# Performance work log

Hardware: AMD Instinct MI355X
Metric: run time of the kernel (lower is better)

The kernel has to match this reference:

```python
import jax, jax.numpy as jnp
import numpy as np
import math

T, B, C, F, H, LF, GF = 1024, 8, 512, 64, 8, 64, 64


def setup_inputs() -> dict:
    key = jax.random.key(0)
    ks = jax.random.split(key, 24)
    s = 0.02  # weight init scale for stability through the recurrence
    rn = lambda k, shp, sc=1.0: jax.random.normal(k, shp, jnp.float32) * sc
    inp = {
        "x": rn(ks[0], (B, T, C)),
        "ln_g": jnp.ones((C,), jnp.float32),
        "ln_b": jnp.zeros((C,), jnp.float32),
        "tl_initial": rn(ks[1], (C,)),
        "tl_premix": jax.random.uniform(ks[2], (C,), jnp.float32),
        "tl_w1": rn(ks[3], (C, LF), s), "tl_b1": jnp.zeros((LF,), jnp.float32),
        "tl_w2": rn(ks[4], (LF, C), s), "tl_b2": jnp.zeros((C,), jnp.float32),
        "bias": jnp.zeros((C,), jnp.float32),
        "gating_res": jax.random.uniform(ks[5], (C,), jnp.float32),
        "g_w1": rn(ks[6], (C, GF), s), "g_b1": jnp.zeros((GF,), jnp.float32),
        "g_w2": rn(ks[7], (GF, C), s), "g_b2": jnp.zeros((C,), jnp.float32),
        "dn_initial": rn(ks[8], (H, F, F)),
        "A_w": rn(ks[9], (H, C, F), s), "A_b": rn(ks[10], (H, F), s),
        "B_w": jnp.zeros((H, C, F), jnp.float32), "B_b": rn(ks[11], (H, F), s),
        "C_w": rn(ks[12], (H, C, F), s), "C_b": rn(ks[13], (H, F), s),
        "D_w": rn(ks[14], (H, C, F), s), "D_b": rn(ks[15], (H, F), s),
        "I_w": rn(ks[16], (H, C, F), s), "I_b": rn(ks[17], (H, F), s),
        "S_w": rn(ks[18], (H, C, F), s), "S_b": rn(ks[19], (H, F), s),
        "O_w": rn(ks[20], (H, F, C), s),
    }
    return inp


def _deltanet_head(y, init_state, Aw, Ab, Bw, Bb, Cw, Cb, Dw, Db, Iw, Ib, Sw, Sb, Ow):
    # y: [T, B, C]; init_state: [F, F]
    f = init_state.shape[-1]
    sf = math.sqrt(f)  # awk_safe
    a = y @ Aw + Ab   # [T,B,F]
    b = y @ Bw + Bb
    c = y @ Cw + Cb
    d = y @ Dw + Db
    i = y @ Iw + Ib
    sel = y @ Sw + Sb
    st0 = jnp.broadcast_to(init_state, (y.shape[1], f, f)).astype(y.dtype)

    def step(st, ins):
        sel_t, a_t, b_t, c_t, d_t, i_t = ins  # each [B,F]
        st = (st * jax.nn.sigmoid(i_t)[:, None, :]
              + jnp.einsum('bij,bj->bi', st, a_t)[:, :, None] * b_t[:, None, :] / sf
              + c_t[:, :, None] * d_t[:, None, :])
        out = jnp.einsum('bf,bfg->bg', sel_t, st)
        return st, out

    st, o = jax.lax.scan(step, st0, (sel, a, b, c, d, i))
    return o @ Ow, st  # [T,B,C]


def reference(x, ln_g, ln_b, tl_initial, tl_premix, tl_w1, tl_b1, tl_w2, tl_b2,
              bias, gating_res, g_w1, g_b1, g_w2, g_b2, dn_initial,
              A_w, A_b, B_w, B_b, C_w, C_b, D_w, D_b, I_w, I_b, S_w, S_b, O_w):
    xt = jnp.swapaxes(x, 0, -2)  # [T, B, C] (time_dim=-2)
    res = xt
    # LayerNorm (eps=1e-5)
    mu = jnp.mean(xt, -1, keepdims=True)
    var = jnp.mean((xt - mu) ** 2, -1, keepdims=True)
    h = (xt - mu) / jnp.sqrt(var + 1e-5) * ln_g + ln_b
    # TokenLerp (state=None -> xf[0]=initial)
    xf = jnp.concatenate([jnp.broadcast_to(tl_initial, (1,) + h.shape[1:]).astype(h.dtype), h[:-1]], axis=0)
    pm = h + (xf - h) * tl_premix
    decide = jax.nn.sigmoid(jax.nn.gelu(pm @ tl_w1 + tl_b1, approximate=False) @ tl_w2 + tl_b2)
    h = h + (xf - h) * decide
    # y starts from bias; heads are chained sequentially (y feeds next head)
    y = jnp.broadcast_to(bias, h.shape).astype(h.dtype)
    for k in range(dn_initial.shape[0]):
        y, _ = _deltanet_head(y, dn_initial[k], A_w[k], A_b[k], B_w[k], B_b[k],
                              C_w[k], C_b[k], D_w[k], D_b[k], I_w[k], I_b[k],
                              S_w[k], S_b[k], O_w[k])
    gate = jax.nn.sigmoid(jax.nn.gelu((y + h * gating_res) @ g_w1 + g_b1, approximate=False) @ g_w2 + g_b2)
    # use_residual=True path: returns res + y (no transpose back, matching source)
    return res + y * gate
```

## Files before the change

kernel.cpp:

```cpp
#include <hip/hip_runtime.h>
#include <hip/hip_bf16.h>

#define T_DIM 1024
#define B_DIM 8
#define C_DIM 512
#define F_DIM 64
#define H_DIM 8
#define CHUNK 32
#define NCHUNK 32

__device__ __forceinline__ float sigmoidf_(float v) { return 1.0f / (1.0f + __expf(-v)); }
__device__ __forceinline__ float geluf_(float v) { return 0.5f * v * (1.0f + erff(v * 0.70710678118654752f)); }
__device__ __forceinline__ float rl_(float v, int l) {
  return __uint_as_float(__builtin_amdgcn_readlane(__float_as_uint(v), l));
}

struct GemmArgs {
  const float* A; const float* W; const float* bias; float* out;
  int M, K, N;
  const float* x; const float* mu; const float* rstd;
  const float* ln_g; const float* ln_b; const float* tl_initial; const float* premix;
  const float* yv; const float* gres;
  float* h2;
  const float* Wg[6]; const float* bg[6];
};

struct AFetch {
  float4 v0, v1, v2, v3, v4;
  float s0, s1, s2, s3;
};

template<int MODE_A>
__device__ __forceinline__ AFetch a_fetch(const GemmArgs& g, int r, int c) {
  AFetch f; f.s0 = f.s1 = f.s2 = f.s3 = 0.f;
  if (MODE_A == 0) {
    f.v0 = *(const float4*)&g.A[r * g.K + c];
  } else if (MODE_A == 1) {
    const int b = r & 7, t = r >> 3;
    f.v0 = *(const float4*)&g.x[(b * T_DIM + t) * C_DIM + c];
    f.s0 = g.mu[r]; f.s1 = g.rstd[r];
    if (t > 0) {
      f.v1 = *(const float4*)&g.x[(b * T_DIM + t - 1) * C_DIM + c];
      f.s2 = g.mu[r - 8]; f.s3 = g.rstd[r - 8];
    } else {
      f.v1 = *(const float4*)&g.tl_initial[c];
    }
    f.v2 = *(const float4*)&g.ln_g[c];
    f.v3 = *(const float4*)&g.ln_b[c];
    f.v4 = *(const float4*)&g.premix[c];
  } else {
    f.v0 = *(const float4*)&g.yv[(r >> 3) * C_DIM + c];
    f.v1 = *(const float4*)&g.h2[r * C_DIM + c];
    f.v2 = *(const float4*)&g.gres[c];
  }
  return f;
}

template<int MODE_A>
__device__ __forceinline__ float4 a_combine(const AFetch& f, int r) {
  if (MODE_A == 0) return f.v0;
  float4 o;
  float* op = (float*)&o;
  const float* xa = (const float*)&f.v0;
  const float* xb = (const float*)&f.v1;
  const float* lg = (const float*)&f.v2;
  const float* lb = (const float*)&f.v3;
  const float* pm = (const float*)&f.v4;
  if (MODE_A == 1) {
    const int t = r >> 3;
    #pragma unroll
    for (int q = 0; q < 4; ++q) {
      float h  = (xa[q] - f.s0) * f.s1 * lg[q] + lb[q];
      float xf = (t == 0) ? xb[q] : (xb[q] - f.s2) * f.s3 * lg[q] + lb[q];
      op[q] = h + (xf - h) * pm[q];
    }
    return o;
  }
  #pragma unroll
  for (int q = 0; q < 4; ++q)
    op[q] = xa[q] + xb[q] * lg[q];
  return o;
}

template<int MODE_B>
__device__ __forceinline__ float4 w_fetch(const GemmArgs& g, int kk, int n0, int tc) {
  if (MODE_B == 1)
    return *(const float4*)&g.Wg[blockIdx.y][kk * 64 + (tc << 2)];
  return *(const float4*)&g.W[kk * g.N + n0 + (tc << 2)];
}

template<int MODE_A, int MODE_B, int EPI>
__global__ __launch_bounds__(256) void gemm_kernel(GemmArgs g) {
  __shared__ float AsT[16][68];
  __shared__ float Bs[16][64];
  const int m0 = blockIdx.x * 64, n0 = blockIdx.y * 64;
  const int tid = threadIdx.x;
  const int tr = tid >> 4, tc = tid & 15;
  const int ai = tid >> 2, aj = (tid & 3) << 2;
  const float scg = (MODE_B == 1 && blockIdx.y == 1) ? 0.125f : 1.0f;
  float acc[4][4] = {};
  AFetch fa = a_fetch<MODE_A>(g, m0 + ai, aj);
  float4 wv = w_fetch<MODE_B>(g, tr, n0, tc);
  for (int k0 = 0; k0 < g.K; k0 += 16) {
    if (k0) __syncthreads();
    const float4 av = a_combine<MODE_A>(fa, m0 + ai);
    AsT[aj + 0][ai] = av.x;
    AsT[aj + 1][ai] = av.y;
    AsT[aj + 2][ai] = av.z;
    AsT[aj + 3][ai] = av.w;
    *(float4*)&Bs[tr][tc << 2] =
        make_float4(wv.x * scg, wv.y * scg, wv.z * scg, wv.w * scg);
    if (k0 + 16 < g.K) {
      fa = a_fetch<MODE_A>(g, m0 + ai, k0 + 16 + aj);
      wv = w_fetch<MODE_B>(g, k0 + 16 + tr, n0, tc);
    }
    __syncthreads();
    #pragma unroll
    for (int kk = 0; kk < 16; ++kk) {
      const float4 a4 = *(const float4*)&AsT[kk][tr << 2];
      const float4 b4 = *(const float4*)&Bs[kk][tc << 2];
      const float avr[4] = {a4.x, a4.y, a4.z, a4.w};
      const float bvr[4] = {b4.x, b4.y, b4.z, b4.w};
      #pragma unroll
      for (int r_ = 0; r_ < 4; ++r_)
        #pragma unroll
        for (int c_ = 0; c_ < 4; ++c_)
          acc[r_][c_] = fmaf(avr[r_], bvr[c_], acc[r_][c_]);
    }
  }
  #pragma unroll
  for (int r_ = 0; r_ < 4; ++r_) {
    const int rr = m0 + (tr << 2) + r_;
    #pragma unroll
    for (int c_ = 0; c_ < 4; ++c_) {
      const int lc = (tc << 2) + c_;
      const int cc = n0 + lc;
      float v = acc[r_][c_];
      if (MODE_B == 1) v += g.bg[blockIdx.y][lc] * scg;
      else if (g.bias) v += g.bias[cc];
      if (EPI == 0) {
        g.out[rr * g.N + cc] = v;
      } else if (EPI == 1) {
        g.out[rr * g.N + cc] = geluf_(v);
      } else if (EPI == 2) {
        float d = sigmoidf_(v);
        const int b = rr & 7, t = rr >> 3;
        float xv = g.x[(b * T_DIM + t) * C_DIM + cc];
        float h = (xv - g.mu[rr]) * g.rstd[rr] * g.ln_g[cc] + g.ln_b[cc];
        float xf;
        if (t == 0) xf = g.tl_initial[cc];
        else {
          float xp = g.x[(b * T_DIM + t - 1) * C_DIM + cc];
          xf = (xp - g.mu[rr - 8]) * g.rstd[rr - 8] * g.ln_g[cc] + g.ln_b[cc];
        }
        g.h2[rr * C_DIM + cc] = h + (xf - h) * d;
      } else {
        float gate = sigmoidf_(v);
        const int b = rr & 7, t = rr >> 3;
        float res = g.x[(b * T_DIM + t) * C_DIM + cc];
        g.out[rr * C_DIM + cc] = res + g.yv[t * C_DIM + cc] * gate;
      }
    }
  }
}

__global__ __launch_bounds__(256) void ln_stats_kernel(const float* __restrict__ x,
                                                       float* __restrict__ mu,
                                                       float* __restrict__ rstd) {
  const int row = blockIdx.x * 4 + (threadIdx.x >> 6);
  const int lane = threadIdx.x & 63;
  const int b = row & 7, t = row >> 3;
  const float* xr = x + (b * T_DIM + t) * C_DIM;
  float4 v0 = *(const float4*)&xr[lane * 8];
  float4 v1 = *(const float4*)&xr[lane * 8 + 4];
  float s  = v0.x + v0.y + v0.z + v0.w + v1.x + v1.y + v1.z + v1.w;
  float s2 = v0.x*v0.x + v0.y*v0.y + v0.z*v0.z + v0.w*v0.w
           + v1.x*v1.x + v1.y*v1.y + v1.z*v1.z + v1.w*v1.w;
  #pragma unroll
  for (int m = 1; m < 64; m <<= 1) { s += __shfl_xor(s, m); s2 += __shfl_xor(s2, m); }
  if (lane == 0) {
    float mean = s * (1.0f / 512.0f);
    float var = s2 * (1.0f / 512.0f) - mean * mean;
    mu[row] = mean;
    rstd[row] = rsqrtf(var + 1e-5f);
  }
}

__global__ __launch_bounds__(256) void yinit_kernel(const float* __restrict__ bias,
                                                    float* __restrict__ y) {
  int i = blockIdx.x * blockDim.x + threadIdx.x;
  y[i] = bias[i & (C_DIM - 1)];
}


__global__ __launch_bounds__(256) void scan_phaseA(const float* __restrict__ PRJ,
                                                   float* __restrict__ chPT,
                                                   float* __restrict__ chS) {
  const int j = blockIdx.x;
  const int tid = threadIdx.x;
  const int ri = tid >> 4, ci = tid & 15;
  float Pm[4][4], Sm[4][4];
  #pragma unroll
  for (int r = 0; r < 4; ++r)
    #pragma unroll
    for (int c = 0; c < 4; ++c) {
      Pm[r][c] = (ri * 4 + r == ci * 4 + c) ? 1.0f : 0.0f;
      Sm[r][c] = 0.0f;
    }
  const float* base = PRJ + j * CHUNK * 384;
  float4 pa = *(const float4*)&base[      ci * 4];
  float4 pb = *(const float4*)&base[ 64 + ci * 4];
  float4 pc = *(const float4*)&base[128 + ri * 4];
  float4 pd = *(const float4*)&base[192 + ci * 4];
  float4 pi = *(const float4*)&base[256 + ci * 4];
  for (int s = 0; s < CHUNK; ++s) {
    float4 na = pa, nb = pb, nc2 = pc, nd = pd, ni = pi;
    if (s + 1 < CHUNK) {
      const float* b2 = base + (s + 1) * 384;
      na  = *(const float4*)&b2[      ci * 4];
      nb  = *(const float4*)&b2[ 64 + ci * 4];
      nc2 = *(const float4*)&b2[128 + ri * 4];
      nd  = *(const float4*)&b2[192 + ci * 4];
      ni  = *(const float4*)&b2[256 + ci * 4];
    }
    const float sg[4] = {sigmoidf_(pi.x), sigmoidf_(pi.y), sigmoidf_(pi.z), sigmoidf_(pi.w)};
    const float aa[4] = {pa.x, pa.y, pa.z, pa.w};
    const float bb[4] = {pb.x, pb.y, pb.z, pb.w};
    const float cv[4] = {pc.x, pc.y, pc.z, pc.w};
    const float dd[4] = {pd.x, pd.y, pd.z, pd.w};
    float rp[4], rs[4];
    #pragma unroll
    for (int r = 0; r < 4; ++r) {
      rp[r] = Pm[r][0]*aa[0] + Pm[r][1]*aa[1] + Pm[r][2]*aa[2] + Pm[r][3]*aa[3];
      rs[r] = Sm[r][0]*aa[0] + Sm[r][1]*aa[1] + Sm[r][2]*aa[2] + Sm[r][3]*aa[3];
    }
    #pragma unroll
    for (int m = 1; m <= 8; m <<= 1) {
      #pragma unroll
      for (int r = 0; r < 4; ++r) {
        rp[r] += __shfl_xor(rp[r], m);
        rs[r] += __shfl_xor(rs[r], m);
      }
    }
    #pragma unroll
    for (int r = 0; r < 4; ++r)
      #pragma unroll
      for (int c = 0; c < 4; ++c) {
        Pm[r][c] = Pm[r][c] * sg[c] + rp[r] * bb[c];
        Sm[r][c] = Sm[r][c] * sg[c] + rs[r] * bb[c] + cv[r] * dd[c];
      }
    pa = na; pb = nb; pc = nc2; pd = nd; pi = ni;
  }
  float* cpT = chPT + j * 4096;
  float* cs  = chS + j * 4096;
  #pragma unroll
  for (int c = 0; c < 4; ++c)
    *(float4*)&cpT[(ci*4+c)*64 + ri*4] =
        make_float4(Pm[0][c], Pm[1][c], Pm[2][c], Pm[3][c]);
  #pragma unroll
  for (int r = 0; r < 4; ++r)
    *(float4*)&cs[(ri*4+r)*64 + ci*4] = make_float4(Sm[r][0], Sm[r][1], Sm[r][2], Sm[r][3]);
}

__device__ __forceinline__ float cstep(const float4 (&P)[16], float sv, float rv) {
  float p0 = 0.f, p1 = 0.f, p2 = 0.f, p3 = 0.f;
  #pragma unroll
  for (int q = 0; q < 16; ++q) {
    p0 = fmaf(rl_(rv, q * 4 + 0), P[q].x, p0);
    p1 = fmaf(rl_(rv, q * 4 + 1), P[q].y, p1);
    p2 = fmaf(rl_(rv, q * 4 + 2), P[q].z, p2);
    p3 = fmaf(rl_(rv, q * 4 + 3), P[q].w, p3);
  }
  return sv + ((p0 + p1) + (p2 + p3));
}

__global__ __launch_bounds__(64) void scan_combine(const float* __restrict__ st0,
                                                   const float* __restrict__ chPT,
                                                   const float* __restrict__ chS,
                                                   float* __restrict__ bnd) {
  const int lane = threadIdx.x;
  const int r = blockIdx.x;
  float rv = st0[r * 64 + lane];
  const float* basePT = chPT + lane * 64;
  const float* baseS  = chS + r * 64 + lane;
  float* bndRL = bnd + r * 64 + lane;
  for (int j = 0; j < NCHUNK; ++j) {
    float4 P[16];
    const float* pp = basePT + j * 4096;
    #pragma unroll
    for (int q = 0; q < 16; ++q) P[q] = *(const float4*)&pp[q * 4];
    const float sv = baseS[j * 4096];
    bndRL[j * 4096] = rv;
    rv = cstep(P, sv, rv);
  }
}

__global__ __launch_bounds__(256) void scan_phaseC(const float* __restrict__ PRJ,
                                                   const float* __restrict__ bnd,
                                                   const float* __restrict__ Ow,
                                                   float* __restrict__ y) {
  __shared__ float olds[CHUNK][4][64];
  __shared__ float osT[64][CHUNK + 1];
  const int j = blockIdx.x;
  const int tid = threadIdx.x;
  const int ri = tid >> 4, ci = tid & 15, w = tid >> 6;
  float st[4][4];
  #pragma unroll
  for (int r = 0; r < 4; ++r) {
    const float4 v = *(const float4*)&bnd[j*4096 + (ri*4+r)*64 + ci*4];
    st[r][0] = v.x; st[r][1] = v.y; st[r][2] = v.z; st[r][3] = v.w;
  }
  const float* base = PRJ + j * CHUNK * 384;
  float4 pa = *(const float4*)&base[      ci * 4];
  float4 pb = *(const float4*)&base[ 64 + ci * 4];
  float4 pc = *(const float4*)&base[128 + ri * 4];
  float4 pd = *(const float4*)&base[192 + ci * 4];
  float4 pi = *(const float4*)&base[256 + ci * 4];
  float4 ps = *(const float4*)&base[320 + ri * 4];
  for (int s = 0; s < CHUNK; ++s) {
    float4 na = pa, nb = pb, nc2 = pc, nd = pd, ni = pi, ns = ps;
    if (s + 1 < CHUNK) {
      const float* b2 = base + (s + 1) * 384;
      na  = *(const float4*)&b2[      ci * 4];
      nb  = *(const float4*)&b2[ 64 + ci * 4];
      nc2 = *(const float4*)&b2[128 + ri * 4];
      nd  = *(const float4*)&b2[192 + ci * 4];
      ni  = *(const float4*)&b2[256 + ci * 4];
      ns  = *(const float4*)&b2[320 + ri * 4];
    }
    const float sg[4] = {sigmoidf_(pi.x), sigmoidf_(pi.y), sigmoidf_(pi.z), sigmoidf_(pi.w)};
    const float aa[4] = {pa.x, pa.y, pa.z, pa.w};
    const float bb[4] = {pb.x, pb.y, pb.z, pb.w};
    const float cv[4] = {pc.x, pc.y, pc.z, pc.w};
    const float dd[4] = {pd.x, pd.y, pd.z, pd.w};
    const float ss[4] = {ps.x, ps.y, ps.z, ps.w};
    float rd[4];
    #pragma unroll
    for (int r = 0; r < 4; ++r)
      rd[r] = st[r][0]*aa[0] + st[r][1]*aa[1] + st[r][2]*aa[2] + st[r][3]*aa[3];
    #pragma unroll
    for (int m = 1; m <= 8; m <<= 1) {
      #pragma unroll
      for (int r = 0; r < 4; ++r) rd[r] += __shfl_xor(rd[r], m);
    }
    float po[4] = {0.f, 0.f, 0.f, 0.f};
    #pragma unroll
    for (int r = 0; r < 4; ++r)
      #pragma unroll
      for (int c = 0; c < 4; ++c) {
        const float nv = st[r][c] * sg[c] + rd[r] * bb[c] + cv[r] * dd[c];
        st[r][c] = nv;
        po[c] = fmaf(ss[r], nv, po[c]);
      }
    #pragma unroll
    for (int c = 0; c < 4; ++c) {
      po[c] += __shfl_xor(po[c], 16);
      po[c] += __shfl_xor(po[c], 32);
    }
    if ((tid & 48) == 0)
      *(float4*)&olds[s][w][ci * 4] = make_float4(po[0], po[1], po[2], po[3]);
    pa = na; pb = nb; pc = nc2; pd = nd; pi = ni; ps = ns;
  }
  __syncthreads();
  #pragma unroll
  for (int e = 0; e < 8; ++e) {
    const int id = tid + 256 * e;
    const int f = id & 63, t = id >> 6;
    osT[f][t] = olds[t][0][f] + olds[t][1][f] + olds[t][2][f] + olds[t][3][f];
  }
  __syncthreads();
  const int c0 = tid << 1;
  float2 acc[CHUNK];
  #pragma unroll
  for (int t = 0; t < CHUNK; ++t) acc[t] = make_float2(0.f, 0.f);
  #pragma unroll 1
  for (int fo = 0; fo < 8; ++fo) {
    float2 ow[8];
    #pragma unroll
    for (int q = 0; q < 8; ++q)
      ow[q] = *(const float2*)&Ow[(fo * 8 + q) * C_DIM + c0];
    #pragma unroll
    for (int q = 0; q < 8; ++q) {
      const int f = fo * 8 + q;
      #pragma unroll
      for (int t8 = 0; t8 < 8; ++t8) {
        const float4 ov = *(const float4*)&osT[f][t8 * 4];
        acc[t8*4+0].x = fmaf(ov.x, ow[q].x, acc[t8*4+0].x);
        acc[t8*4+0].y = fmaf(ov.x, ow[q].y, acc[t8*4+0].y);
        acc[t8*4+1].x = fmaf(ov.y, ow[q].x, acc[t8*4+1].x);
        acc[t8*4+1].y = fmaf(ov.y, ow[q].y, acc[t8*4+1].y);
        acc[t8*4+2].x = fmaf(ov.z, ow[q].x, acc[t8*4+2].x);
        acc[t8*4+2].y = fmaf(ov.z, ow[q].y, acc[t8*4+2].y);
        acc[t8*4+3].x = fmaf(ov.w, ow[q].x, acc[t8*4+3].x);
        acc[t8*4+3].y = fmaf(ov.w, ow[q].y, acc[t8*4+3].y);
      }
    }
  }
  #pragma unroll
  for (int t = 0; t < CHUNK; ++t)
    *(float2*)&y[(j * CHUNK + t) * C_DIM + c0] = acc[t];
}

extern "C" void kernel_launch(void* const* d_in, const int* in_sizes, int n_in,
                              void* d_out, int out_size, void* d_ws, size_t ws_size,
                              hipStream_t stream) {
  const float* x       = (const float*)d_in[0];
  const float* ln_g    = (const float*)d_in[1];
  const float* ln_b    = (const float*)d_in[2];
  const float* tl_init = (const float*)d_in[3];
  const float* premix  = (const float*)d_in[4];
  const float* tl_w1   = (const float*)d_in[5];
  const float* tl_b1   = (const float*)d_in[6];
  const float* tl_w2   = (const float*)d_in[7];
  const float* tl_b2   = (const float*)d_in[8];
  const float* bias    = (const float*)d_in[9];
  const float* gres    = (const float*)d_in[10];
  const float* g_w1    = (const float*)d_in[11];
  const float* g_b1    = (const float*)d_in[12];
  const float* g_w2    = (const float*)d_in[13];
  const float* g_b2    = (const float*)d_in[14];
  const float* dn_init = (const float*)d_in[15];
  const float* A_w     = (const float*)d_in[16];
  const float* A_b     = (const float*)d_in[17];
  const float* B_w     = (const float*)d_in[18];
  const float* B_b     = (const float*)d_in[19];
  const float* C_w     = (const float*)d_in[20];
  const float* C_b     = (const float*)d_in[21];
  const float* D_w     = (const float*)d_in[22];
  const float* D_b     = (const float*)d_in[23];
  const float* I_w     = (const float*)d_in[24];
  const float* I_b     = (const float*)d_in[25];
  const float* S_w     = (const float*)d_in[26];
  const float* S_b     = (const float*)d_in[27];
  const float* O_w     = (const float*)d_in[28];

  float* ws      = (float*)d_ws;
  float* mu      = ws;
  float* rstd    = mu + 8192;
  float* hidden1 = rstd + 8192;
  float* y       = hidden1 + 524288;
  float* PRJ     = y + 524288;
  float* chPT    = PRJ + 393216;
  float* chS     = chPT + 131072;
  float* bnd     = chS + 131072;
  float* h2      = (float*)d_out;

  ln_stats_kernel<<<2048, 256, 0, stream>>>(x, mu, rstd);
  yinit_kernel<<<2048, 256, 0, stream>>>(bias, y);

  GemmArgs ga = {};
  ga.x = x; ga.mu = mu; ga.rstd = rstd; ga.ln_g = ln_g; ga.ln_b = ln_b;
  ga.tl_initial = tl_init; ga.premix = premix; ga.gres = gres; ga.h2 = h2;

  {
    GemmArgs g = ga; g.W = tl_w1; g.bias = tl_b1; g.out = hidden1;
    g.M = 8192; g.K = 512; g.N = 64;
    gemm_kernel<1, 0, 1><<<dim3(128, 1), 256, 0, stream>>>(g);
  }
  {
    GemmArgs g = ga; g.A = hidden1; g.W = tl_w2; g.bias = tl_b2;
    g.M = 8192; g.K = 64; g.N = 512;
    gemm_kernel<0, 0, 2><<<dim3(128, 8), 256, 0, stream>>>(g);
  }

  for (int k = 0; k < H_DIM; ++k) {
    {
      GemmArgs g = ga; g.A = y; g.out = PRJ; g.M = 1024; g.K = 512; g.N = 384;
      const int woff = k * C_DIM * F_DIM, boff = k * F_DIM;
      g.Wg[0] = A_w + woff; g.Wg[1] = B_w + woff; g.Wg[2] = C_w + woff;
      g.Wg[3] = D_w + woff; g.Wg[4] = I_w + woff; g.Wg[5] = S_w + woff;
      g.bg[0] = A_b + boff; g.bg[1] = B_b + boff; g.bg[2] = C_b + boff;
      g.bg[3] = D_b + boff; g.bg[4] = I_b + boff; g.bg[5] = S_b + boff;
      gemm_kernel<0, 1, 0><<<dim3(16, 6), 256, 0, stream>>>(g);
    }
    scan_phaseA<<<NCHUNK, 256, 0, stream>>>(PRJ, chPT, chS);
    scan_combine<<<64, 64, 0, stream>>>(dn_init + k * 4096, chPT, chS, bnd);
    scan_phaseC<<<NCHUNK, 256, 0, stream>>>(PRJ, bnd, O_w + k * F_DIM * C_DIM, y);
  }

  {
    GemmArgs g = ga; g.yv = y; g.W = g_w1; g.bias = g_b1; g.out = hidden1;
    g.M = 8192; g.K = 512; g.N = 64;
    gemm_kernel<2, 0, 1><<<dim3(128, 1), 256, 0, stream>>>(g);
  }
  {
    GemmArgs g = ga; g.yv = y; g.A = hidden1; g.W = g_w2; g.bias = g_b2;
    g.out = (float*)d_out; g.M = 8192; g.K = 64; g.N = 512;
    gemm_kernel<0, 0, 3><<<dim3(128, 8), 256, 0, stream>>>(g);
  }
}
```

Baseline: 968.0 us.

## Fuse per-head projection and chunked scan phases into one cooperative persistent kernel

Replaces the 32 per-head kernel launches (projection GEMM, chunk scan, combine, output phase) and the y-init kernel with a single cooperative kernel of 96 blocks that loops over heads and uses grid-wide syncs between phases. This is meant to remove launch overhead and the gaps between small, latency-bound kernels in the sequential head chain. In exchange, grid.sync costs are added, and many blocks sit idle during the scan phases. The generic GEMM template also drops its multi-weight mode.

```diff
diff --git a/kernel.cpp b/kernel.cpp
--- a/kernel.cpp
+++ b/kernel.cpp
@@ -1,5 +1,8 @@
 #include <hip/hip_runtime.h>
 #include <hip/hip_bf16.h>
+#include <hip/hip_cooperative_groups.h>
+
+namespace cg = cooperative_groups;
 
 #define T_DIM 1024
 #define B_DIM 8
@@ -22,7 +25,6 @@
   const float* ln_g; const float* ln_b; const float* tl_initial; const float* premix;
   const float* yv; const float* gres;
   float* h2;
-  const float* Wg[6]; const float* bg[6];
 };
 
 struct AFetch {
@@ -82,14 +84,7 @@
   return o;
 }
 
-template<int MODE_B>
-__device__ __forceinline__ float4 w_fetch(const GemmArgs& g, int kk, int n0, int tc) {
-  if (MODE_B == 1)
-    return *(const float4*)&g.Wg[blockIdx.y][kk * 64 + (tc << 2)];
-  return *(const float4*)&g.W[kk * g.N + n0 + (tc << 2)];
-}
-
-template<int MODE_A, int MODE_B, int EPI>
+template<int MODE_A, int EPI>
 __global__ __launch_bounds__(256) void gemm_kernel(GemmArgs g) {
   __shared__ float AsT[16][68];
   __shared__ float Bs[16][64];
@@ -97,10 +92,9 @@
   const int tid = threadIdx.x;
   const int tr = tid >> 4, tc = tid & 15;
   const int ai = tid >> 2, aj = (tid & 3) << 2;
-  const float scg = (MODE_B == 1 && blockIdx.y == 1) ? 0.125f : 1.0f;
   float acc[4][4] = {};
   AFetch fa = a_fetch<MODE_A>(g, m0 + ai, aj);
-  float4 wv = w_fetch<MODE_B>(g, tr, n0, tc);
+  float4 wv = *(const float4*)&g.W[tr * g.N + n0 + (tc << 2)];
   for (int k0 = 0; k0 < g.K; k0 += 16) {
     if (k0) __syncthreads();
     const float4 av = a_combine<MODE_A>(fa, m0 + ai);
@@ -108,11 +102,10 @@
     AsT[aj + 1][ai] = av.y;
     AsT[aj + 2][ai] = av.z;
     AsT[aj + 3][ai] = av.w;
-    *(float4*)&Bs[tr][tc << 2] =
-        make_float4(wv.x * scg, wv.y * scg, wv.z * scg, wv.w * scg);
+    *(float4*)&Bs[tr][tc << 2] = wv;
     if (k0 + 16 < g.K) {
       fa = a_fetch<MODE_A>(g, m0 + ai, k0 + 16 + aj);
-      wv = w_fetch<MODE_B>(g, k0 + 16 + tr, n0, tc);
+      wv = *(const float4*)&g.W[(k0 + 16 + tr) * g.N + n0 + (tc << 2)];
     }
     __syncthreads();
     #pragma unroll
@@ -133,14 +126,10 @@
     const int rr = m0 + (tr << 2) + r_;
     #pragma unroll
     for (int c_ = 0; c_ < 4; ++c_) {
-      const int lc = (tc << 2) + c_;
-      const int cc = n0 + lc;
+      const int cc = n0 + (tc << 2) + c_;
       float v = acc[r_][c_];
-      if (MODE_B == 1) v += g.bg[blockIdx.y][lc] * scg;
-      else if (g.bias) v += g.bias[cc];
-      if (EPI == 0) {
-        g.out[rr * g.N + cc] = v;
-      } else if (EPI == 1) {
+      if (g.bias) v += g.bias[cc];
+      if (EPI == 1) {
         g.out[rr * g.N + cc] = geluf_(v);
       } else if (EPI == 2) {
         float d = sigmoidf_(v);
@@ -186,82 +175,6 @@
   }
 }
 
-__global__ __launch_bounds__(256) void yinit_kernel(const float* __restrict__ bias,
-                                                    float* __restrict__ y) {
-  int i = blockIdx.x * blockDim.x + threadIdx.x;
-  y[i] = bias[i & (C_DIM - 1)];
-}
-
-
-__global__ __launch_bounds__(256) void scan_phaseA(const float* __restrict__ PRJ,
-                                                   float* __restrict__ chPT,
-                                                   float* __restrict__ chS) {
-  const int j = blockIdx.x;
-  const int tid = threadIdx.x;
-  const int ri = tid >> 4, ci = tid & 15;
-  float Pm[4][4], Sm[4][4];
-  #pragma unroll
-  for (int r = 0; r < 4; ++r)
-    #pragma unroll
-    for (int c = 0; c < 4; ++c) {
-      Pm[r][c] = (ri * 4 + r == ci * 4 + c) ? 1.0f : 0.0f;
-      Sm[r][c] = 0.0f;
-    }
-  const float* base = PRJ + j * CHUNK * 384;
-  float4 pa = *(const float4*)&base[      ci * 4];
-  float4 pb = *(const float4*)&base[ 64 + ci * 4];
-  float4 pc = *(const float4*)&base[128 + ri * 4];
-  float4 pd = *(const float4*)&base[192 + ci * 4];
-  float4 pi = *(const float4*)&base[256 + ci * 4];
-  for (int s = 0; s < CHUNK; ++s) {
-    float4 na = pa, nb = pb, nc2 = pc, nd = pd, ni = pi;
-    if (s + 1 < CHUNK) {
-      const float* b2 = base + (s + 1) * 384;
-      na  = *(const float4*)&b2[      ci * 4];
-      nb  = *(const float4*)&b2[ 64 + ci * 4];
-      nc2 = *(const float4*)&b2[128 + ri * 4];
-      nd  = *(const float4*)&b2[192 + ci * 4];
-      ni  = *(const float4*)&b2[256 + ci * 4];
-    }
-    const float sg[4] = {sigmoidf_(pi.x), sigmoidf_(pi.y), sigmoidf_(pi.z), sigmoidf_(pi.w)};
-    const float aa[4] = {pa.x, pa.y, pa.z, pa.w};
-    const float bb[4] = {pb.x, pb.y, pb.z, pb.w};
-    const float cv[4] = {pc.x, pc.y, pc.z, pc.w};
-    const float dd[4] = {pd.x, pd.y, pd.z, pd.w};
-    float rp[4], rs[4];
-    #pragma unroll
-    for (int r = 0; r < 4; ++r) {
-      rp[r] = Pm[r][0]*aa[0] + Pm[r][1]*aa[1] + Pm[r][2]*aa[2] + Pm[r][3]*aa[3];
-      rs[r] = Sm[r][0]*aa[0] + Sm[r][1]*aa[1] + Sm[r][2]*aa[2] + Sm[r][3]*aa[3];
-    }
-    #pragma unroll
-    for (int m = 1; m <= 8; m <<= 1) {
-      #pragma unroll
-      for (int r = 0; r < 4; ++r) {
-        rp[r] += __shfl_xor(rp[r], m);
-        rs[r] += __shfl_xor(rs[r], m);
-      }
-    }
-    #pragma unroll
-    for (int r = 0; r < 4; ++r)
-      #pragma unroll
-      for (int c = 0; c < 4; ++c) {
-        Pm[r][c] = Pm[r][c] * sg[c] + rp[r] * bb[c];
-        Sm[r][c] = Sm[r][c] * sg[c] + rs[r] * bb[c] + cv[r] * dd[c];
-      }
-    pa = na; pb = nb; pc = nc2; pd = nd; pi = ni;
-  }
-  float* cpT = chPT + j * 4096;
-  float* cs  = chS + j * 4096;
-  #pragma unroll
-  for (int c = 0; c < 4; ++c)
-    *(float4*)&cpT[(ci*4+c)*64 + ri*4] =
-        make_float4(Pm[0][c], Pm[1][c], Pm[2][c], Pm[3][c]);
-  #pragma unroll
-  for (int r = 0; r < 4; ++r)
-    *(float4*)&cs[(ri*4+r)*64 + ci*4] = make_float4(Sm[r][0], Sm[r][1], Sm[r][2], Sm[r][3]);
-}
-
 __device__ __forceinline__ float cstep(const float4 (&P)[16], float sv, float rv) {
   float p0 = 0.f, p1 = 0.f, p2 = 0.f, p3 = 0.f;
   #pragma unroll
@@ -274,131 +187,265 @@
   return sv + ((p0 + p1) + (p2 + p3));
 }
 
-__global__ __launch_bounds__(64) void scan_combine(const float* __restrict__ st0,
-                                                   const float* __restrict__ chPT,
-                                                   const float* __restrict__ chS,
-                                                   float* __restrict__ bnd) {
-  const int lane = threadIdx.x;
-  const int r = blockIdx.x;
-  float rv = st0[r * 64 + lane];
-  const float* basePT = chPT + lane * 64;
-  const float* baseS  = chS + r * 64 + lane;
-  float* bndRL = bnd + r * 64 + lane;
-  for (int j = 0; j < NCHUNK; ++j) {
-    float4 P[16];
-    const float* pp = basePT + j * 4096;
-    #pragma unroll
-    for (int q = 0; q < 16; ++q) P[q] = *(const float4*)&pp[q * 4];
-    const float sv = baseS[j * 4096];
-    bndRL[j * 4096] = rv;
-    rv = cstep(P, sv, rv);
-  }
-}
-
-__global__ __launch_bounds__(256) void scan_phaseC(const float* __restrict__ PRJ,
-                                                   const float* __restrict__ bnd,
-                                                   const float* __restrict__ Ow,
-                                                   float* __restrict__ y) {
-  __shared__ float olds[CHUNK][4][64];
-  __shared__ float osT[64][CHUNK + 1];
-  const int j = blockIdx.x;
+struct HeadArgs {
+  const float* bias;
+  const float* dn_init;
+  const float* Ws[6];
+  const float* bs[6];
+  const float* Ow;
+  float* y; float* PRJ; float* chPT; float* chS; float* bnd;
+};
+
+__global__ __launch_bounds__(256) void head_loop_kernel(HeadArgs a) {
+  cg::grid_group grid = cg::this_grid();
+  __shared__ float smem[10304];
+  const int blk = blockIdx.x;
   const int tid = threadIdx.x;
-  const int ri = tid >> 4, ci = tid & 15, w = tid >> 6;
-  float st[4][4];
-  #pragma unroll
-  for (int r = 0; r < 4; ++r) {
-    const float4 v = *(const float4*)&bnd[j*4096 + (ri*4+r)*64 + ci*4];
-    st[r][0] = v.x; st[r][1] = v.y; st[r][2] = v.z; st[r][3] = v.w;
-  }
-  const float* base = PRJ + j * CHUNK * 384;
-  float4 pa = *(const float4*)&base[      ci * 4];
-  float4 pb = *(const float4*)&base[ 64 + ci * 4];
-  float4 pc = *(const float4*)&base[128 + ri * 4];
-  float4 pd = *(const float4*)&base[192 + ci * 4];
-  float4 pi = *(const float4*)&base[256 + ci * 4];
-  float4 ps = *(const float4*)&base[320 + ri * 4];
-  for (int s = 0; s < CHUNK; ++s) {
-    float4 na = pa, nb = pb, nc2 = pc, nd = pd, ni = pi, ns = ps;
-    if (s + 1 < CHUNK) {
-      const float* b2 = base + (s + 1) * 384;
-      na  = *(const float4*)&b2[      ci * 4];
-      nb  = *(const float4*)&b2[ 64 + ci * 4];
-      nc2 = *(const float4*)&b2[128 + ri * 4];
-      nd  = *(const float4*)&b2[192 + ci * 4];
-      ni  = *(const float4*)&b2[256 + ci * 4];
-      ns  = *(const float4*)&b2[320 + ri * 4];
-    }
-    const float sg[4] = {sigmoidf_(pi.x), sigmoidf_(pi.y), sigmoidf_(pi.z), sigmoidf_(pi.w)};
-    const float aa[4] = {pa.x, pa.y, pa.z, pa.w};
-    const float bb[4] = {pb.x, pb.y, pb.z, pb.w};
-    const float cv[4] = {pc.x, pc.y, pc.z, pc.w};
-    const float dd[4] = {pd.x, pd.y, pd.z, pd.w};
-    const float ss[4] = {ps.x, ps.y, ps.z, ps.w};
-    float rd[4];
-    #pragma unroll
-    for (int r = 0; r < 4; ++r)
-      rd[r] = st[r][0]*aa[0] + st[r][1]*aa[1] + st[r][2]*aa[2] + st[r][3]*aa[3];
-    #pragma unroll
-    for (int m = 1; m <= 8; m <<= 1) {
-      #pragma unroll
-      for (int r = 0; r < 4; ++r) rd[r] += __shfl_xor(rd[r], m);
-    }
-    float po[4] = {0.f, 0.f, 0.f, 0.f};
-    #pragma unroll
-    for (int r = 0; r < 4; ++r)
-      #pragma unroll
-      for (int c = 0; c < 4; ++c) {
-        const float nv = st[r][c] * sg[c] + rd[r] * bb[c] + cv[r] * dd[c];
-        st[r][c] = nv;
-        po[c] = fmaf(ss[r], nv, po[c]);
-      }
-    #pragma unroll
-    for (int c = 0; c < 4; ++c) {
-      po[c] += __shfl_xor(po[c], 16);
-      po[c] += __shfl_xor(po[c], 32);
-    }
-    if ((tid & 48) == 0)
-      *(float4*)&olds[s][w][ci * 4] = make_float4(po[0], po[1], po[2], po[3]);
-    pa = na; pb = nb; pc = nc2; pd = nd; pi = ni; ps = ns;
-  }
-  __syncthreads();
-  #pragma unroll
-  for (int e = 0; e < 8; ++e) {
-    const int id = tid + 256 * e;
-    const int f = id & 63, t = id >> 6;
-    osT[f][t] = olds[t][0][f] + olds[t][1][f] + olds[t][2][f] + olds[t][3][f];
-  }
-  __syncthreads();
-  const int c0 = tid << 1;
-  float2 acc[CHUNK];
-  #pragma unroll
-  for (int t = 0; t < CHUNK; ++t) acc[t] = make_float2(0.f, 0.f);
-  #pragma unroll 1
-  for (int fo = 0; fo < 8; ++fo) {
-    float2 ow[8];
-    #pragma unroll
-    for (int q = 0; q < 8; ++q)
-      ow[q] = *(const float2*)&Ow[(fo * 8 + q) * C_DIM + c0];
-    #pragma unroll
-    for (int q = 0; q < 8; ++q) {
-      const int f = fo * 8 + q;
-      #pragma unroll
-      for (int t8 = 0; t8 < 8; ++t8) {
-        const float4 ov = *(const float4*)&osT[f][t8 * 4];
-        acc[t8*4+0].x = fmaf(ov.x, ow[q].x, acc[t8*4+0].x);
-        acc[t8*4+0].y = fmaf(ov.x, ow[q].y, acc[t8*4+0].y);
-        acc[t8*4+1].x = fmaf(ov.y, ow[q].x, acc[t8*4+1].x);
-        acc[t8*4+1].y = fmaf(ov.y, ow[q].y, acc[t8*4+1].y);
-        acc[t8*4+2].x = fmaf(ov.z, ow[q].x, acc[t8*4+2].x);
-        acc[t8*4+2].y = fmaf(ov.z, ow[q].y, acc[t8*4+2].y);
-        acc[t8*4+3].x = fmaf(ov.w, ow[q].x, acc[t8*4+3].x);
-        acc[t8*4+3].y = fmaf(ov.w, ow[q].y, acc[t8*4+3].y);
-      }
-    }
-  }
-  #pragma unroll
-  for (int t = 0; t < CHUNK; ++t)
-    *(float2*)&y[(j * CHUNK + t) * C_DIM + c0] = acc[t];
+
+  for (int i = blk * 256 + tid; i < T_DIM * C_DIM; i += 96 * 256)
+    a.y[i] = a.bias[i & (C_DIM - 1)];
+  grid.sync();
+
+  for (int k = 0; k < H_DIM; ++k) {
+    {
+      const int m0 = (blk & 15) * 64, grp = blk >> 4;
+      float (*AsT)[68] = (float(*)[68])smem;
+      float (*Bs)[64] = (float(*)[64])(smem + 16 * 68);
+      const int tr = tid >> 4, tc = tid & 15;
+      const int ai = tid >> 2, aj = (tid & 3) << 2;
+      const float* W = a.Ws[grp] + k * (C_DIM * F_DIM);
+      const float scg = (grp == 1) ? 0.125f : 1.0f;
+      float acc[4][4] = {};
+      float4 fa = *(const float4*)&a.y[(m0 + ai) * C_DIM + aj];
+      float4 wv = *(const float4*)&W[tr * 64 + (tc << 2)];
+      for (int k0 = 0; k0 < C_DIM; k0 += 16) {
+        if (k0) __syncthreads();
+        AsT[aj + 0][ai] = fa.x; AsT[aj + 1][ai] = fa.y;
+        AsT[aj + 2][ai] = fa.z; AsT[aj + 3][ai] = fa.w;
+        *(float4*)&Bs[tr][tc << 2] =
+            make_float4(wv.x * scg, wv.y * scg, wv.z * scg, wv.w * scg);
+        if (k0 + 16 < C_DIM) {
+          fa = *(const float4*)&a.y[(m0 + ai) * C_DIM + k0 + 16 + aj];
+          wv = *(const float4*)&W[(k0 + 16 + tr) * 64 + (tc << 2)];
+        }
+        __syncthreads();
+        #pragma unroll
+        for (int kk = 0; kk < 16; ++kk) {
+          const float4 a4 = *(const float4*)&AsT[kk][tr << 2];
+          const float4 b4 = *(const float4*)&Bs[kk][tc << 2];
+          const float avr[4] = {a4.x, a4.y, a4.z, a4.w};
+          const float bvr[4] = {b4.x, b4.y, b4.z, b4.w};
+          #pragma unroll
+          for (int r_ = 0; r_ < 4; ++r_)
+            #pragma unroll
+            for (int c_ = 0; c_ < 4; ++c_)
+              acc[r_][c_] = fmaf(avr[r_], bvr[c_], acc[r_][c_]);
+        }
+      }
+      const float* bb = a.bs[grp] + k * F_DIM;
+      #pragma unroll
+      for (int r_ = 0; r_ < 4; ++r_) {
+        const int rr = m0 + (tr << 2) + r_;
+        #pragma unroll
+        for (int c_ = 0; c_ < 4; ++c_) {
+          const int lc = (tc << 2) + c_;
+          a.PRJ[rr * 384 + grp * 64 + lc] = acc[r_][c_] + bb[lc] * scg;
+        }
+      }
+    }
+    grid.sync();
+
+    if (blk < NCHUNK) {
+      const int j = blk;
+      const int ri = tid >> 4, ci = tid & 15;
+      float Pm[4][4], Sm[4][4];
+      #pragma unroll
+      for (int r = 0; r < 4; ++r)
+        #pragma unroll
+        for (int c = 0; c < 4; ++c) {
+          Pm[r][c] = (ri * 4 + r == ci * 4 + c) ? 1.0f : 0.0f;
+          Sm[r][c] = 0.0f;
+        }
+      const float* base = a.PRJ + j * CHUNK * 384;
+      float4 pa = *(const float4*)&base[      ci * 4];
+      float4 pb = *(const float4*)&base[ 64 + ci * 4];
+      float4 pc = *(const float4*)&base[128 + ri * 4];
+      float4 pd = *(const float4*)&base[192 + ci * 4];
+      float4 pi = *(const float4*)&base[256 + ci * 4];
+      for (int s = 0; s < CHUNK; ++s) {
+        float4 na = pa, nb = pb, nc2 = pc, nd = pd, ni = pi;
+        if (s + 1 < CHUNK) {
+          const float* b2 = base + (s + 1) * 384;
+          na  = *(const float4*)&b2[      ci * 4];
+          nb  = *(const float4*)&b2[ 64 + ci * 4];
+          nc2 = *(const float4*)&b2[128 + ri * 4];
+          nd  = *(const float4*)&b2[192 + ci * 4];
+          ni  = *(const float4*)&b2[256 + ci * 4];
+        }
+        const float sg[4] = {sigmoidf_(pi.x), sigmoidf_(pi.y), sigmoidf_(pi.z), sigmoidf_(pi.w)};
+        const float aa[4] = {pa.x, pa.y, pa.z, pa.w};
+        const float bb2[4] = {pb.x, pb.y, pb.z, pb.w};
+        const float cv[4] = {pc.x, pc.y, pc.z, pc.w};
+        const float dd[4] = {pd.x, pd.y, pd.z, pd.w};
+        float rp[4], rs[4];
+        #pragma unroll
+        for (int r = 0; r < 4; ++r) {
+          rp[r] = Pm[r][0]*aa[0] + Pm[r][1]*aa[1] + Pm[r][2]*aa[2] + Pm[r][3]*aa[3];
+          rs[r] = Sm[r][0]*aa[0] + Sm[r][1]*aa[1] + Sm[r][2]*aa[2] + Sm[r][3]*aa[3];
+        }
+        #pragma unroll
+        for (int m = 1; m <= 8; m <<= 1) {
+          #pragma unroll
+          for (int r = 0; r < 4; ++r) {
+            rp[r] += __shfl_xor(rp[r], m);
+            rs[r] += __shfl_xor(rs[r], m);
+          }
+        }
+        #pragma unroll
+        for (int r = 0; r < 4; ++r)
+          #pragma unroll
+          for (int c = 0; c < 4; ++c) {
+            Pm[r][c] = Pm[r][c] * sg[c] + rp[r] * bb2[c];
+            Sm[r][c] = Sm[r][c] * sg[c] + rs[r] * bb2[c] + cv[r] * dd[c];
+          }
+        pa = na; pb = nb; pc = nc2; pd = nd; pi = ni;
+      }
+      float* cpT = a.chPT + j * 4096;
+      float* cs  = a.chS + j * 4096;
+      #pragma unroll
+      for (int c = 0; c < 4; ++c)
+        *(float4*)&cpT[(ci*4+c)*64 + ri*4] =
+            make_float4(Pm[0][c], Pm[1][c], Pm[2][c], Pm[3][c]);
+      #pragma unroll
+      for (int r = 0; r < 4; ++r)
+        *(float4*)&cs[(ri*4+r)*64 + ci*4] =
+            make_float4(Sm[r][0], Sm[r][1], Sm[r][2], Sm[r][3]);
+    }
+    grid.sync();
+
+    if (blk < 16) {
+      const int lane = tid & 63;
+      const int r = blk * 4 + (tid >> 6);
+      float rv = a.dn_init[k * 4096 + r * 64 + lane];
+      const float* basePT = a.chPT + lane * 64;
+      const float* baseS  = a.chS + r * 64 + lane;
+      float* bndRL = a.bnd + r * 64 + lane;
+      for (int j = 0; j < NCHUNK; ++j) {
+        float4 P[16];
+        const float* pp = basePT + j * 4096;
+        #pragma unroll
+        for (int q = 0; q < 16; ++q) P[q] = *(const float4*)&pp[q * 4];
+        const float sv = baseS[j * 4096];
+        bndRL[j * 4096] = rv;
+        rv = cstep(P, sv, rv);
+      }
+    }
+    grid.sync();
+
+    if (blk < NCHUNK) {
+      const int j = blk;
+      float (*olds)[4][64] = (float(*)[4][64])smem;
+      float (*osT)[CHUNK + 1] = (float(*)[CHUNK + 1])(smem + 8192);
+      const int ri = tid >> 4, ci = tid & 15, w = tid >> 6;
+      const float* Ow = a.Ow + k * F_DIM * C_DIM;
+      float st[4][4];
+      #pragma unroll
+      for (int r = 0; r < 4; ++r) {
+        const float4 v = *(const float4*)&a.bnd[j*4096 + (ri*4+r)*64 + ci*4];
+        st[r][0] = v.x; st[r][1] = v.y; st[r][2] = v.z; st[r][3] = v.w;
+      }
+      const float* base = a.PRJ + j * CHUNK * 384;
+      float4 pa = *(const float4*)&base[      ci * 4];
+      float4 pb = *(const float4*)&base[ 64 + ci * 4];
+      float4 pc = *(const float4*)&base[128 + ri * 4];
+      float4 pd = *(const float4*)&base[192 + ci * 4];
+      float4 pi = *(const float4*)&base[256 + ci * 4];
+      float4 ps = *(const float4*)&base[320 + ri * 4];
+      for (int s = 0; s < CHUNK; ++s) {
+        float4 na = pa, nb = pb, nc2 = pc, nd = pd, ni = pi, ns = ps;
+        if (s + 1 < CHUNK) {
+          const float* b2 = base + (s + 1) * 384;
+          na  = *(const float4*)&b2[      ci * 4];
+          nb  = *(const float4*)&b2[ 64 + ci * 4];
+          nc2 = *(const float4*)&b2[128 + ri * 4];
+          nd  = *(const float4*)&b2[192 + ci * 4];
+          ni  = *(const float4*)&b2[256 + ci * 4];
+          ns  = *(const float4*)&b2[320 + ri * 4];
+        }
+        const float sg[4] = {sigmoidf_(pi.x), sigmoidf_(pi.y), sigmoidf_(pi.z), sigmoidf_(pi.w)};
+        const float aa[4] = {pa.x, pa.y, pa.z, pa.w};
+        const float bb2[4] = {pb.x, pb.y, pb.z, pb.w};
+        const float cv[4] = {pc.x, pc.y, pc.z, pc.w};
+        const float dd[4] = {pd.x, pd.y, pd.z, pd.w};
+        const float ss[4] = {ps.x, ps.y, ps.z, ps.w};
+        float rd[4];
+        #pragma unroll
+        for (int r = 0; r < 4; ++r)
+          rd[r] = st[r][0]*aa[0] + st[r][1]*aa[1] + st[r][2]*aa[2] + st[r][3]*aa[3];
+        #pragma unroll
+        for (int m = 1; m <= 8; m <<= 1) {
+          #pragma unroll
+          for (int r = 0; r < 4; ++r) rd[r] += __shfl_xor(rd[r], m);
+        }
+        float po[4] = {0.f, 0.f, 0.f, 0.f};
+        #pragma unroll
+        for (int r = 0; r < 4; ++r)
+          #pragma unroll
+          for (int c = 0; c < 4; ++c) {
+            const float nv = st[r][c] * sg[c] + rd[r] * bb2[c] + cv[r] * dd[c];
+            st[r][c] = nv;
+            po[c] = fmaf(ss[r], nv, po[c]);
+          }
+        #pragma unroll
+        for (int c = 0; c < 4; ++c) {
+          po[c] += __shfl_xor(po[c], 16);
+          po[c] += __shfl_xor(po[c], 32);
+        }
+        if ((tid & 48) == 0)
+          *(float4*)&olds[s][w][ci * 4] = make_float4(po[0], po[1], po[2], po[3]);
+        pa = na; pb = nb; pc = nc2; pd = nd; pi = ni; ps = ns;
+      }
+      __syncthreads();
+      #pragma unroll
+      for (int e = 0; e < 8; ++e) {
+        const int id = tid + 256 * e;
+        const int f = id & 63, t = id >> 6;
+        osT[f][t] = olds[t][0][f] + olds[t][1][f] + olds[t][2][f] + olds[t][3][f];
+      }
+      __syncthreads();
+      const int c0 = tid << 1;
+      float2 acc[CHUNK];
+      #pragma unroll
+      for (int t = 0; t < CHUNK; ++t) acc[t] = make_float2(0.f, 0.f);
+      #pragma unroll 1
+      for (int fo = 0; fo < 8; ++fo) {
+        float2 ow[8];
+        #pragma unroll
+        for (int q = 0; q < 8; ++q)
+          ow[q] = *(const float2*)&Ow[(fo * 8 + q) * C_DIM + c0];
+        #pragma unroll
+        for (int q = 0; q < 8; ++q) {
+          const int f = fo * 8 + q;
+          #pragma unroll
+          for (int t8 = 0; t8 < 8; ++t8) {
+            const float4 ov = *(const float4*)&osT[f][t8 * 4];
+            acc[t8*4+0].x = fmaf(ov.x, ow[q].x, acc[t8*4+0].x);
+            acc[t8*4+0].y = fmaf(ov.x, ow[q].y, acc[t8*4+0].y);
+            acc[t8*4+1].x = fmaf(ov.y, ow[q].x, acc[t8*4+1].x);
+            acc[t8*4+1].y = fmaf(ov.y, ow[q].y, acc[t8*4+1].y);
+            acc[t8*4+2].x = fmaf(ov.z, ow[q].x, acc[t8*4+2].x);
+            acc[t8*4+2].y = fmaf(ov.z, ow[q].y, acc[t8*4+2].y);
+            acc[t8*4+3].x = fmaf(ov.w, ow[q].x, acc[t8*4+3].x);
+            acc[t8*4+3].y = fmaf(ov.w, ow[q].y, acc[t8*4+3].y);
+          }
+        }
+      }
+      #pragma unroll
+      for (int t = 0; t < CHUNK; ++t)
+        *(float2*)&a.y[(j * CHUNK + t) * C_DIM + c0] = acc[t];
+    }
+    grid.sync();
+  }
 }
 
 extern "C" void kernel_launch(void* const* d_in, const int* in_sizes, int n_in,
@@ -446,7 +493,6 @@
   float* h2      = (float*)d_out;
 
   ln_stats_kernel<<<2048, 256, 0, stream>>>(x, mu, rstd);
-  yinit_kernel<<<2048, 256, 0, stream>>>(bias, y);
 
   GemmArgs ga = {};
   ga.x = x; ga.mu = mu; ga.rstd = rstd; ga.ln_g = ln_g; ga.ln_b = ln_b;
@@ -455,37 +501,35 @@
   {
     GemmArgs g = ga; g.W = tl_w1; g.bias = tl_b1; g.out = hidden1;
     g.M = 8192; g.K = 512; g.N = 64;
-    gemm_kernel<1, 0, 1><<<dim3(128, 1), 256, 0, stream>>>(g);
+    gemm_kernel<1, 1><<<dim3(128, 1), 256, 0, stream>>>(g);
   }
   {
     GemmArgs g = ga; g.A = hidden1; g.W = tl_w2; g.bias = tl_b2;
     g.M = 8192; g.K = 64; g.N = 512;
-    gemm_kernel<0, 0, 2><<<dim3(128, 8), 256, 0, stream>>>(g);
-  }
-
-  for (int k = 0; k < H_DIM; ++k) {
-    {
-      GemmArgs g = ga; g.A = y; g.out = PRJ; g.M = 1024; g.K = 512; g.N = 384;
-      const int woff = k * C_DIM * F_DIM, boff = k * F_DIM;
-      g.Wg[0] = A_w + woff; g.Wg[1] = B_w + woff; g.Wg[2] = C_w + woff;
-      g.Wg[3] = D_w + woff; g.Wg[4] = I_w + woff; g.Wg[5] = S_w + woff;
-      g.bg[0] = A_b + boff; g.bg[1] = B_b + boff; g.bg[2] = C_b + boff;
-      g.bg[3] = D_b + boff; g.bg[4] = I_b + boff; g.bg[5] = S_b + boff;
-      gemm_kernel<0, 1, 0><<<dim3(16, 6), 256, 0, stream>>>(g);
-    }
-    scan_phaseA<<<NCHUNK, 256, 0, stream>>>(PRJ, chPT, chS);
-    scan_combine<<<64, 64, 0, stream>>>(dn_init + k * 4096, chPT, chS, bnd);
-    scan_phaseC<<<NCHUNK, 256, 0, stream>>>(PRJ, bnd, O_w + k * F_DIM * C_DIM, y);
+    gemm_kernel<0, 2><<<dim3(128, 8), 256, 0, stream>>>(g);
+  }
+
+  {
+    HeadArgs ha;
+    ha.bias = bias; ha.dn_init = dn_init;
+    ha.Ws[0] = A_w; ha.Ws[1] = B_w; ha.Ws[2] = C_w;
+    ha.Ws[3] = D_w; ha.Ws[4] = I_w; ha.Ws[5] = S_w;
+    ha.bs[0] = A_b; ha.bs[1] = B_b; ha.bs[2] = C_b;
+    ha.bs[3] = D_b; ha.bs[4] = I_b; ha.bs[5] = S_b;
+    ha.Ow = O_w; ha.y = y; ha.PRJ = PRJ; ha.chPT = chPT; ha.chS = chS; ha.bnd = bnd;
+    void* kargs[] = { &ha };
+    hipLaunchCooperativeKernel((const void*)head_loop_kernel, dim3(96), dim3(256),
+                               kargs, 0, stream);
   }
 
   {
     GemmArgs g = ga; g.yv = y; g.W = g_w1; g.bias = g_b1; g.out = hidden1;
     g.M = 8192; g.K = 512; g.N = 64;
-    gemm_kernel<2, 0, 1><<<dim3(128, 1), 256, 0, stream>>>(g);
+    gemm_kernel<2, 1><<<dim3(128, 1), 256, 0, stream>>>(g);
   }
   {
     GemmArgs g = ga; g.yv = y; g.A = hidden1; g.W = g_w2; g.bias = g_b2;
     g.out = (float*)d_out; g.M = 8192; g.K = 64; g.N = 512;
-    gemm_kernel<0, 0, 3><<<dim3(128, 8), 256, 0, stream>>>(g);
-  }
-}
+    gemm_kernel<0, 3><<<dim3(128, 8), 256, 0, stream>>>(g);
+  }
+}
```

After: 1.751 ms. +80.9%, slower.
